# Kernel tuning notes

Hardware: AMD Instinct MI355X
Metric: run time of the kernel (lower is better)

The kernel has to match this reference:

```python
import jax, jax.numpy as jnp
import numpy as np

NEG_FILL = -1000.0

def setup_inputs() -> dict:
    key = jax.random.key(0)
    k1, k2, k3, k4 = jax.random.split(key, 4)
    B, N, D = 16, 2048, 64
    q = jax.random.normal(k1, (B, N, D), dtype=jnp.float32)
    k = jax.random.normal(k2, (B, N, D), dtype=jnp.float32)
    v = jax.random.normal(k3, (B, N, D), dtype=jnp.float32)
    mask = jax.random.randint(k4, (B, N, N), 0, 2) == 1
    return {"q": q, "k": k, "v": v, "mask": mask}

def reference(q, k, v, mask):
    # Faithful to the torch module: scale by sqrt(seq_len) = len(q[0])**0.5,
    # masked positions set to -1000.0, softmax over dim=1 (NOT the last dim).
    seq_len = q.shape[1]
    scores = jnp.einsum('bnd,bmd->bnm', q, k) / jnp.sqrt(jnp.float32(seq_len))
    scores = jnp.where(mask, NEG_FILL, scores)
    attn = jax.nn.softmax(scores, axis=1)  # dim=1 as in nn.Softmax(dim=1)
    out = jnp.einsum('bnm,bmd->bnd', attn, v)
    return out
```

## Files before the change

kernel.cpp:

```cpp
#include <hip/hip_runtime.h>
#include <hip/hip_bf16.h>


#define B_ 16
#define N_ 2048
#define D_ 64
#define SCALE 0.022097086912079608f
#define NWORD (N_ / 32)
#define MCH 4
#define NCH 4

typedef __attribute__((ext_vector_type(8))) short bf16x8;
typedef __attribute__((ext_vector_type(4))) float f32x4;

static __device__ __forceinline__ short f2bf(float x) {
  unsigned u = __float_as_uint(x);
  return (short)((u + 0x7FFF + ((u >> 16) & 1)) >> 16);
}

static __device__ __forceinline__ bf16x8 load8(const short* p) {
  return *reinterpret_cast<const bf16x8*>(p);
}

static __device__ __forceinline__ bf16x8 load8f(const float* p) {
  const f32x4 a = *reinterpret_cast<const f32x4*>(p);
  const f32x4 b = *reinterpret_cast<const f32x4*>(p + 4);
  bf16x8 r;
  r[0] = f2bf(a[0]); r[1] = f2bf(a[1]); r[2] = f2bf(a[2]); r[3] = f2bf(a[3]);
  r[4] = f2bf(b[0]); r[5] = f2bf(b[1]); r[6] = f2bf(b[2]); r[7] = f2bf(b[3]);
  return r;
}

__global__ __launch_bounds__(256) void pack_mask(const int* __restrict__ mask,
                                                 unsigned* __restrict__ bits) {
  const size_t w = (size_t)blockIdx.x * 256 + threadIdx.x;
  const int4* p = reinterpret_cast<const int4*>(mask) + w * 8;
  unsigned r = 0;
#pragma unroll
  for (int j = 0; j < 8; ++j) {
    const int4 x = p[j];
    r |= (x.x ? 1u : 0u) << (j * 4);
    r |= (x.y ? 1u : 0u) << (j * 4 + 1);
    r |= (x.z ? 1u : 0u) << (j * 4 + 2);
    r |= (x.w ? 1u : 0u) << (j * 4 + 3);
  }
  bits[w] = r;
}

__global__ __launch_bounds__(256) void cvt_bf16(const float* __restrict__ q,
                                                const float* __restrict__ k,
                                                short* __restrict__ qb,
                                                short* __restrict__ kb) {
  const size_t i = ((size_t)blockIdx.x * 256 + threadIdx.x) * 8;
  const float* src = blockIdx.y ? k : q;
  short* dst = blockIdx.y ? kb : qb;
  *reinterpret_cast<bf16x8*>(dst + i) = load8f(src + i);
}

__global__ __launch_bounds__(256) void colsum_kernel(
    const short* __restrict__ qb, const short* __restrict__ kb,
    const unsigned* __restrict__ bits, float* __restrict__ csp) {
  const int b = blockIdx.x;
  const int wave = threadIdx.x >> 6;
  const int lane = threadIdx.x & 63;
  const int l15 = lane & 15;
  const int lhi = lane >> 4;
  const int m0 = blockIdx.y * 128 + wave * 32;
  const int wword = m0 >> 5;
  const int nbase = blockIdx.z * (N_ / NCH);

  const short* qbb = qb + (size_t)b * N_ * D_;
  const short* kbb = kb + (size_t)b * N_ * D_;
  const unsigned* bitsb = bits + (size_t)b * N_ * NWORD;

  bf16x8 kf[2][2];
#pragma unroll
  for (int cg = 0; cg < 2; ++cg) {
    kf[cg][0] = load8(kbb + (m0 + cg * 16 + l15) * D_ + lhi * 8);
    kf[cg][1] = load8(kbb + (m0 + cg * 16 + l15) * D_ + 32 + lhi * 8);
  }

  float part[2] = {0.f, 0.f};
  for (int n0 = nbase; n0 < nbase + N_ / NCH; n0 += 16) {
    const bf16x8 qf0 = load8(qbb + (n0 + l15) * D_ + lhi * 8);
    const bf16x8 qf1 = load8(qbb + (n0 + l15) * D_ + 32 + lhi * 8);
    unsigned w[4];
#pragma unroll
    for (int r = 0; r < 4; ++r)
      w[r] = bitsb[(n0 + lhi * 4 + r) * NWORD + wword];
#pragma unroll
    for (int cg = 0; cg < 2; ++cg) {
      f32x4 acc = {0.f, 0.f, 0.f, 0.f};
      acc = __builtin_amdgcn_mfma_f32_16x16x32_bf16(qf0, kf[cg][0], acc, 0, 0, 0);
      acc = __builtin_amdgcn_mfma_f32_16x16x32_bf16(qf1, kf[cg][1], acc, 0, 0, 0);
#pragma unroll
      for (int r = 0; r < 4; ++r) {
        const unsigned msk = (w[r] >> (cg * 16 + l15)) & 1u;
        part[cg] += msk ? 0.f : __expf(acc[r] * SCALE);
      }
    }
  }
#pragma unroll
  for (int cg = 0; cg < 2; ++cg) {
    float p = part[cg];
    p += __shfl_xor(p, 16, 64);
    p += __shfl_xor(p, 32, 64);
    if (lane < 16)
      csp[(size_t)blockIdx.z * B_ * N_ + (size_t)b * N_ + m0 + cg * 16 + l15] =
          p;
  }
}

__global__ __launch_bounds__(256) void vprep_kernel(
    const float* __restrict__ v, const float* __restrict__ csp,
    short* __restrict__ vt) {
  const int b = blockIdx.x;
  const int m0 = blockIdx.y * 64;
  const int tid = threadIdx.x;
  __shared__ float lds[64][65];

  const float* vb = v + (size_t)b * N_ * D_;
#pragma unroll
  for (int pass = 0; pass < 4; ++pass) {
    const int mloc = pass * 16 + (tid >> 4);
    const int d4 = (tid & 15) * 4;
    const f32x4 x = *reinterpret_cast<const f32x4*>(vb + (m0 + mloc) * D_ + d4);
    float cs = 0.f;
#pragma unroll
    for (int z = 0; z < NCH; ++z)
      cs += csp[(size_t)z * B_ * N_ + (size_t)b * N_ + m0 + mloc];
    const float ic = 1.0f / cs;
    lds[mloc][d4 + 0] = x[0] * ic;
    lds[mloc][d4 + 1] = x[1] * ic;
    lds[mloc][d4 + 2] = x[2] * ic;
    lds[mloc][d4 + 3] = x[3] * ic;
  }
  __syncthreads();
  const int d = tid >> 2;
  const int seg = tid & 3;
  bf16x8 o0, o1;
#pragma unroll
  for (int i = 0; i < 8; ++i) o0[i] = f2bf(lds[seg * 16 + i][d]);
#pragma unroll
  for (int i = 0; i < 8; ++i) o1[i] = f2bf(lds[seg * 16 + 8 + i][d]);
  short* dst = vt + (size_t)b * D_ * N_ + (size_t)d * N_ + m0 + seg * 16;
  *reinterpret_cast<bf16x8*>(dst) = o0;
  *reinterpret_cast<bf16x8*>(dst + 8) = o1;
}

__global__ __launch_bounds__(256) void attn_out_kernel(
    const short* __restrict__ qb, const short* __restrict__ kb,
    const short* __restrict__ vt, const unsigned* __restrict__ bits,
    float* __restrict__ outp) {
  const int b = blockIdx.x;
  const int wave = threadIdx.x >> 6;
  const int lane = threadIdx.x & 63;
  const int l15 = lane & 15;
  const int lhi = lane >> 4;
  const int n0 = blockIdx.y * 64 + wave * 16;
  const int mbase = blockIdx.z * (N_ / MCH);

  const short* qbb = qb + (size_t)b * N_ * D_;
  const short* kbb = kb + (size_t)b * N_ * D_;
  const short* vtb = vt + (size_t)b * D_ * N_;
  const unsigned* bitsb = bits + (size_t)b * N_ * NWORD;

  const bf16x8 qf0 = load8(qbb + (n0 + l15) * D_ + lhi * 8);
  const bf16x8 qf1 = load8(qbb + (n0 + l15) * D_ + 32 + lhi * 8);

  __shared__ __align__(16) short pbuf[4][16][32];

  f32x4 oacc[4];
#pragma unroll
  for (int d = 0; d < 4; ++d) oacc[d] = (f32x4){0.f, 0.f, 0.f, 0.f};

  for (int m0 = mbase; m0 < mbase + N_ / MCH; m0 += 32) {
    unsigned w[4];
#pragma unroll
    for (int r = 0; r < 4; ++r)
      w[r] = bitsb[(n0 + lhi * 4 + r) * NWORD + (m0 >> 5)];
#pragma unroll
    for (int cg = 0; cg < 2; ++cg) {
      const int mc = m0 + cg * 16;
      const bf16x8 kf0 = load8(kbb + (mc + l15) * D_ + lhi * 8);
      const bf16x8 kf1 = load8(kbb + (mc + l15) * D_ + 32 + lhi * 8);
      f32x4 acc = {0.f, 0.f, 0.f, 0.f};
      acc = __builtin_amdgcn_mfma_f32_16x16x32_bf16(qf0, kf0, acc, 0, 0, 0);
      acc = __builtin_amdgcn_mfma_f32_16x16x32_bf16(qf1, kf1, acc, 0, 0, 0);
#pragma unroll
      for (int r = 0; r < 4; ++r) {
        const unsigned msk = (w[r] >> (cg * 16 + l15)) & 1u;
        const float p = msk ? 0.f : __expf(acc[r] * SCALE);
        pbuf[wave][lhi * 4 + r][cg * 16 + l15] = f2bf(p);
      }
    }
    __builtin_amdgcn_wave_barrier();
    asm volatile("s_waitcnt lgkmcnt(0)" ::: "memory");
    const bf16x8 pa =
        *reinterpret_cast<const bf16x8*>(&pbuf[wave][l15][lhi * 8]);
#pragma unroll
    for (int dsub = 0; dsub < 4; ++dsub) {
      const bf16x8 vf =
          load8(vtb + (size_t)(dsub * 16 + l15) * N_ + m0 + lhi * 8);
      oacc[dsub] =
          __builtin_amdgcn_mfma_f32_16x16x32_bf16(pa, vf, oacc[dsub], 0, 0, 0);
    }
    __builtin_amdgcn_wave_barrier();
  }

  float* dst = outp + (size_t)blockIdx.z * B_ * N_ * D_ + (size_t)b * N_ * D_;
#pragma unroll
  for (int dsub = 0; dsub < 4; ++dsub)
#pragma unroll
    for (int r = 0; r < 4; ++r)
      dst[(size_t)(n0 + lhi * 4 + r) * D_ + dsub * 16 + l15] = oacc[dsub][r];
}

__global__ __launch_bounds__(256) void reduce_out(const float* __restrict__ outp,
                                                  float* __restrict__ out) {
  const size_t i = ((size_t)blockIdx.x * 256 + threadIdx.x) * 4;
  f32x4 s = *reinterpret_cast<const f32x4*>(outp + i);
#pragma unroll
  for (int z = 1; z < MCH; ++z) {
    const f32x4 x =
        *reinterpret_cast<const f32x4*>(outp + (size_t)z * B_ * N_ * D_ + i);
    s[0] += x[0]; s[1] += x[1]; s[2] += x[2]; s[3] += x[3];
  }
  *reinterpret_cast<f32x4*>(out + i) = s;
}

__global__ __launch_bounds__(256) void colsum_fb(
    const float* __restrict__ q, const float* __restrict__ k,
    const int* __restrict__ mask, float* __restrict__ colsum) {
  const int b = blockIdx.x;
  const int wave = threadIdx.x >> 6;
  const int lane = threadIdx.x & 63;
  const int l15 = lane & 15;
  const int lhi = lane >> 4;
  const int m0 = blockIdx.y * 64 + wave * 16;
  const float* qbp = q + (size_t)b * N_ * D_;
  const float* kbp = k + (size_t)b * N_ * D_;
  const int* maskb = mask + (size_t)b * N_ * N_;
  const bf16x8 kf0 = load8f(kbp + (m0 + l15) * D_ + lhi * 8);
  const bf16x8 kf1 = load8f(kbp + (m0 + l15) * D_ + 32 + lhi * 8);
  float partial = 0.f;
  for (int n0 = 0; n0 < N_; n0 += 16) {
    bf16x8 qf0 = load8f(qbp + (n0 + l15) * D_ + lhi * 8);
    bf16x8 qf1 = load8f(qbp + (n0 + l15) * D_ + 32 + lhi * 8);
    f32x4 acc = {0.f, 0.f, 0.f, 0.f};
    acc = __builtin_amdgcn_mfma_f32_16x16x32_bf16(qf0, kf0, acc, 0, 0, 0);
    acc = __builtin_amdgcn_mfma_f32_16x16x32_bf16(qf1, kf1, acc, 0, 0, 0);
#pragma unroll
    for (int r = 0; r < 4; ++r) {
      const int n = n0 + lhi * 4 + r;
      partial +=
          maskb[(size_t)n * N_ + m0 + l15] ? 0.f : __expf(acc[r] * SCALE);
    }
  }
  partial += __shfl_xor(partial, 16, 64);
  partial += __shfl_xor(partial, 32, 64);
  if (lane < 16) colsum[(size_t)b * N_ + m0 + l15] = partial;
}

__global__ __launch_bounds__(256) void attn_out_fb(
    const float* __restrict__ q, const float* __restrict__ k,
    const float* __restrict__ v, const int* __restrict__ mask,
    const float* __restrict__ colsum, float* __restrict__ out) {
  const int b = blockIdx.x;
  const int wave = threadIdx.x >> 6;
  const int lane = threadIdx.x & 63;
  const int l15 = lane & 15;
  const int lhi = lane >> 4;
  const int n0 = blockIdx.y * 64 + wave * 16;
  const float* qbp = q + (size_t)b * N_ * D_;
  const float* kbp = k + (size_t)b * N_ * D_;
  const float* vbp = v + (size_t)b * N_ * D_;
  const int* maskb = mask + (size_t)b * N_ * N_;
  const float* csb = colsum + (size_t)b * N_;
  const bf16x8 qf0 = load8f(qbp + (n0 + l15) * D_ + lhi * 8);
  const bf16x8 qf1 = load8f(qbp + (n0 + l15) * D_ + 32 + lhi * 8);
  __shared__ __align__(16) short pbuf[4][16][32];
  f32x4 oacc[4];
#pragma unroll
  for (int d = 0; d < 4; ++d) oacc[d] = (f32x4){0.f, 0.f, 0.f, 0.f};
  for (int m0 = 0; m0 < N_; m0 += 32) {
#pragma unroll
    for (int cg = 0; cg < 2; ++cg) {
      const int mc = m0 + cg * 16;
      bf16x8 kf0 = load8f(kbp + (mc + l15) * D_ + lhi * 8);
      bf16x8 kf1 = load8f(kbp + (mc + l15) * D_ + 32 + lhi * 8);
      f32x4 acc = {0.f, 0.f, 0.f, 0.f};
      acc = __builtin_amdgcn_mfma_f32_16x16x32_bf16(qf0, kf0, acc, 0, 0, 0);
      acc = __builtin_amdgcn_mfma_f32_16x16x32_bf16(qf1, kf1, acc, 0, 0, 0);
      const float ic = 1.0f / csb[mc + l15];
#pragma unroll
      for (int r = 0; r < 4; ++r) {
        const int n = n0 + lhi * 4 + r;
        const float p = maskb[(size_t)n * N_ + mc + l15]
                            ? 0.f
                            : __expf(acc[r] * SCALE) * ic;
        pbuf[wave][lhi * 4 + r][cg * 16 + l15] = f2bf(p);
      }
    }
    __syncthreads();
    const bf16x8 pa =
        *reinterpret_cast<const bf16x8*>(&pbuf[wave][l15][lhi * 8]);
#pragma unroll
    for (int dsub = 0; dsub < 4; ++dsub) {
      bf16x8 vf;
#pragma unroll
      for (int j = 0; j < 8; ++j)
        vf[j] = f2bf(vbp[(m0 + lhi * 8 + j) * D_ + dsub * 16 + l15]);
      oacc[dsub] =
          __builtin_amdgcn_mfma_f32_16x16x32_bf16(pa, vf, oacc[dsub], 0, 0, 0);
    }
    __syncthreads();
  }
#pragma unroll
  for (int dsub = 0; dsub < 4; ++dsub)
#pragma unroll
    for (int r = 0; r < 4; ++r)
      out[(size_t)b * N_ * D_ + (size_t)(n0 + lhi * 4 + r) * D_ + dsub * 16 +
          l15] = oacc[dsub][r];
}

extern "C" void kernel_launch(void* const* d_in, const int* in_sizes, int n_in,
                              void* d_out, int out_size, void* d_ws,
                              size_t ws_size, hipStream_t stream) {
  const float* q = (const float*)d_in[0];
  const float* k = (const float*)d_in[1];
  const float* v = (const float*)d_in[2];
  const int* mask = (const int*)d_in[3];
  float* out = (float*)d_out;

  const size_t MB = 1024 * 1024;
  const size_t cs_off = 0;
  const size_t qb_off = cs_off + NCH * (size_t)B_ * N_ * 4;
  const size_t kb_off = qb_off + 4 * MB;
  const size_t vt_off = kb_off + 4 * MB;
  const size_t bt_off = vt_off + 4 * MB;
  const size_t op_off = bt_off + 8 * MB;
  const size_t need = op_off + (size_t)MCH * B_ * N_ * D_ * 4;

  if (ws_size >= need) {
    float* csp = (float*)((char*)d_ws + cs_off);
    short* qbf = (short*)((char*)d_ws + qb_off);
    short* kbf = (short*)((char*)d_ws + kb_off);
    short* vt = (short*)((char*)d_ws + vt_off);
    unsigned* bits = (unsigned*)((char*)d_ws + bt_off);
    float* outp = (float*)((char*)d_ws + op_off);

    pack_mask<<<(B_ * N_ * NWORD) / 256, 256, 0, stream>>>(mask, bits);
    cvt_bf16<<<dim3((B_ * N_ * D_) / (256 * 8), 2), 256, 0, stream>>>(
        q, k, qbf, kbf);
    colsum_kernel<<<dim3(B_, N_ / 128, NCH), 256, 0, stream>>>(qbf, kbf, bits,
                                                               csp);
    vprep_kernel<<<dim3(B_, N_ / 64), 256, 0, stream>>>(v, csp, vt);
    attn_out_kernel<<<dim3(B_, N_ / 64, MCH), 256, 0, stream>>>(qbf, kbf, vt,
                                                                bits, outp);
    reduce_out<<<(B_ * N_ * D_) / (256 * 4), 256, 0, stream>>>(outp, out);
  } else {
    float* colsum = (float*)d_ws;
    colsum_fb<<<dim3(B_, N_ / 64), 256, 0, stream>>>(q, k, mask, colsum);
    attn_out_fb<<<dim3(B_, N_ / 64), 256, 0, stream>>>(q, k, v, mask, colsum,
                                                       out);
  }
}
```

Baseline: 542.4 us.

## Fuse mask packing into colsum kernel with transposed 16-bit mask layout

Removes the separate pack_mask kernel: colsum now reads the int mask directly and uses wave ballots to write a transposed bitmask in 16-bit words, indexed by key-block then query row. attn_out reads this transposed mask with a single 8-byte load per 16-column group instead of four scattered word loads. MCH drops from 4 to 2, halving the partial-output buffer and reduce traffic but also halving grid parallelism. The wave barriers in attn_out become full block __syncthreads, which adds cross-wave synchronisation even though each wave uses its own pbuf slice.

After: 573.3 us. 5.7% more time.

```diff
diff --git a/kernel.cpp b/kernel.cpp
--- a/kernel.cpp
+++ b/kernel.cpp
@@ -6,8 +6,7 @@
 #define N_ 2048
 #define D_ 64
 #define SCALE 0.022097086912079608f
-#define NWORD (N_ / 32)
-#define MCH 4
+#define MCH 2
 #define NCH 4
 
 typedef __attribute__((ext_vector_type(8))) short bf16x8;
@@ -29,22 +28,6 @@
   r[0] = f2bf(a[0]); r[1] = f2bf(a[1]); r[2] = f2bf(a[2]); r[3] = f2bf(a[3]);
   r[4] = f2bf(b[0]); r[5] = f2bf(b[1]); r[6] = f2bf(b[2]); r[7] = f2bf(b[3]);
   return r;
-}
-
-__global__ __launch_bounds__(256) void pack_mask(const int* __restrict__ mask,
-                                                 unsigned* __restrict__ bits) {
-  const size_t w = (size_t)blockIdx.x * 256 + threadIdx.x;
-  const int4* p = reinterpret_cast<const int4*>(mask) + w * 8;
-  unsigned r = 0;
-#pragma unroll
-  for (int j = 0; j < 8; ++j) {
-    const int4 x = p[j];
-    r |= (x.x ? 1u : 0u) << (j * 4);
-    r |= (x.y ? 1u : 0u) << (j * 4 + 1);
-    r |= (x.z ? 1u : 0u) << (j * 4 + 2);
-    r |= (x.w ? 1u : 0u) << (j * 4 + 3);
-  }
-  bits[w] = r;
 }
 
 __global__ __launch_bounds__(256) void cvt_bf16(const float* __restrict__ q,
@@ -57,21 +40,22 @@
   *reinterpret_cast<bf16x8*>(dst + i) = load8f(src + i);
 }
 
-__global__ __launch_bounds__(256) void colsum_kernel(
+__global__ __launch_bounds__(256) void colsum_pack(
     const short* __restrict__ qb, const short* __restrict__ kb,
-    const unsigned* __restrict__ bits, float* __restrict__ csp) {
+    const int* __restrict__ mask, unsigned short* __restrict__ bitsT,
+    float* __restrict__ csp) {
   const int b = blockIdx.x;
   const int wave = threadIdx.x >> 6;
   const int lane = threadIdx.x & 63;
   const int l15 = lane & 15;
   const int lhi = lane >> 4;
   const int m0 = blockIdx.y * 128 + wave * 32;
-  const int wword = m0 >> 5;
   const int nbase = blockIdx.z * (N_ / NCH);
 
   const short* qbb = qb + (size_t)b * N_ * D_;
   const short* kbb = kb + (size_t)b * N_ * D_;
-  const unsigned* bitsb = bits + (size_t)b * N_ * NWORD;
+  const int* maskb = mask + (size_t)b * N_ * N_;
+  unsigned short* bitsTb = bitsT + (size_t)b * 128 * N_;
 
   bf16x8 kf[2][2];
 #pragma unroll
@@ -84,18 +68,20 @@
   for (int n0 = nbase; n0 < nbase + N_ / NCH; n0 += 16) {
     const bf16x8 qf0 = load8(qbb + (n0 + l15) * D_ + lhi * 8);
     const bf16x8 qf1 = load8(qbb + (n0 + l15) * D_ + 32 + lhi * 8);
-    unsigned w[4];
-#pragma unroll
-    for (int r = 0; r < 4; ++r)
-      w[r] = bitsb[(n0 + lhi * 4 + r) * NWORD + wword];
 #pragma unroll
     for (int cg = 0; cg < 2; ++cg) {
       f32x4 acc = {0.f, 0.f, 0.f, 0.f};
       acc = __builtin_amdgcn_mfma_f32_16x16x32_bf16(qf0, kf[cg][0], acc, 0, 0, 0);
       acc = __builtin_amdgcn_mfma_f32_16x16x32_bf16(qf1, kf[cg][1], acc, 0, 0, 0);
+      const int wc = (m0 >> 4) + cg;
 #pragma unroll
       for (int r = 0; r < 4; ++r) {
-        const unsigned msk = (w[r] >> (cg * 16 + l15)) & 1u;
+        const int n = n0 + lhi * 4 + r;
+        const int msk = maskb[(size_t)n * N_ + m0 + cg * 16 + l15];
+        const unsigned long long bal = __ballot(msk != 0);
+        if (l15 == 0)
+          bitsTb[(size_t)wc * N_ + n0 + 4 * lhi + r] =
+              (unsigned short)(bal >> (lhi * 16));
         part[cg] += msk ? 0.f : __expf(acc[r] * SCALE);
       }
     }
@@ -150,7 +136,7 @@
 
 __global__ __launch_bounds__(256) void attn_out_kernel(
     const short* __restrict__ qb, const short* __restrict__ kb,
-    const short* __restrict__ vt, const unsigned* __restrict__ bits,
+    const short* __restrict__ vt, const unsigned short* __restrict__ bitsT,
     float* __restrict__ outp) {
   const int b = blockIdx.x;
   const int wave = threadIdx.x >> 6;
@@ -163,7 +149,7 @@
   const short* qbb = qb + (size_t)b * N_ * D_;
   const short* kbb = kb + (size_t)b * N_ * D_;
   const short* vtb = vt + (size_t)b * D_ * N_;
-  const unsigned* bitsb = bits + (size_t)b * N_ * NWORD;
+  const unsigned short* bitsTb = bitsT + (size_t)b * 128 * N_;
 
   const bf16x8 qf0 = load8(qbb + (n0 + l15) * D_ + lhi * 8);
   const bf16x8 qf1 = load8(qbb + (n0 + l15) * D_ + 32 + lhi * 8);
@@ -175,27 +161,25 @@
   for (int d = 0; d < 4; ++d) oacc[d] = (f32x4){0.f, 0.f, 0.f, 0.f};
 
   for (int m0 = mbase; m0 < mbase + N_ / MCH; m0 += 32) {
-    unsigned w[4];
-#pragma unroll
-    for (int r = 0; r < 4; ++r)
-      w[r] = bitsb[(n0 + lhi * 4 + r) * NWORD + (m0 >> 5)];
 #pragma unroll
     for (int cg = 0; cg < 2; ++cg) {
       const int mc = m0 + cg * 16;
       const bf16x8 kf0 = load8(kbb + (mc + l15) * D_ + lhi * 8);
       const bf16x8 kf1 = load8(kbb + (mc + l15) * D_ + 32 + lhi * 8);
+      const uint2 u2 = *reinterpret_cast<const uint2*>(
+          bitsTb + (size_t)((mc) >> 4) * N_ + n0 + lhi * 4);
       f32x4 acc = {0.f, 0.f, 0.f, 0.f};
       acc = __builtin_amdgcn_mfma_f32_16x16x32_bf16(qf0, kf0, acc, 0, 0, 0);
       acc = __builtin_amdgcn_mfma_f32_16x16x32_bf16(qf1, kf1, acc, 0, 0, 0);
 #pragma unroll
       for (int r = 0; r < 4; ++r) {
-        const unsigned msk = (w[r] >> (cg * 16 + l15)) & 1u;
-        const float p = msk ? 0.f : __expf(acc[r] * SCALE);
+        const unsigned half = (r < 2 ? u2.x : u2.y) >> ((r & 1) * 16);
+        const unsigned bit = (half >> l15) & 1u;
+        const float p = bit ? 0.f : __expf(acc[r] * SCALE);
         pbuf[wave][lhi * 4 + r][cg * 16 + l15] = f2bf(p);
       }
     }
-    __builtin_amdgcn_wave_barrier();
-    asm volatile("s_waitcnt lgkmcnt(0)" ::: "memory");
+    __syncthreads();
     const bf16x8 pa =
         *reinterpret_cast<const bf16x8*>(&pbuf[wave][l15][lhi * 8]);
 #pragma unroll
@@ -205,7 +189,7 @@
       oacc[dsub] =
           __builtin_amdgcn_mfma_f32_16x16x32_bf16(pa, vf, oacc[dsub], 0, 0, 0);
     }
-    __builtin_amdgcn_wave_barrier();
+    __syncthreads();
   }
 
   float* dst = outp + (size_t)blockIdx.z * B_ * N_ * D_ + (size_t)b * N_ * D_;
@@ -347,17 +331,16 @@
     short* qbf = (short*)((char*)d_ws + qb_off);
     short* kbf = (short*)((char*)d_ws + kb_off);
     short* vt = (short*)((char*)d_ws + vt_off);
-    unsigned* bits = (unsigned*)((char*)d_ws + bt_off);
+    unsigned short* bitsT = (unsigned short*)((char*)d_ws + bt_off);
     float* outp = (float*)((char*)d_ws + op_off);
 
-    pack_mask<<<(B_ * N_ * NWORD) / 256, 256, 0, stream>>>(mask, bits);
     cvt_bf16<<<dim3((B_ * N_ * D_) / (256 * 8), 2), 256, 0, stream>>>(
         q, k, qbf, kbf);
-    colsum_kernel<<<dim3(B_, N_ / 128, NCH), 256, 0, stream>>>(qbf, kbf, bits,
-                                                               csp);
+    colsum_pack<<<dim3(B_, N_ / 128, NCH), 256, 0, stream>>>(qbf, kbf, mask,
+                                                             bitsT, csp);
     vprep_kernel<<<dim3(B_, N_ / 64), 256, 0, stream>>>(v, csp, vt);
     attn_out_kernel<<<dim3(B_, N_ / 64, MCH), 256, 0, stream>>>(qbf, kbf, vt,
-                                                                bits, outp);
+                                                                bitsT, outp);
     reduce_out<<<(B_ * N_ * D_) / (256 * 4), 256, 0, stream>>>(outp, out);
   } else {
     float* colsum = (float*)d_ws;
```
